# Kernel optimization log

Hardware: AMD Instinct MI355X
Metric: run time of the kernel (lower is better)

Reference implementation:

```python
import jax, jax.numpy as jnp
import numpy as np

D_MODEL = 1024
NUM_HEADS = 16
HEAD_DIM = D_MODEL // NUM_HEADS
B, TQ, TK = 4, 2048, 2048


def setup_inputs() -> dict:
    key = jax.random.key(0)
    ks = jax.random.split(key, 6)
    s = 1.0 / np.sqrt(D_MODEL)
    return {
        "x_q": jax.random.normal(ks[0], (B, TQ, D_MODEL), dtype=jnp.float32),
        "x_kv": jax.random.normal(ks[1], (B, TK, D_MODEL), dtype=jnp.float32),
        "attn_mask": jnp.zeros((TQ, TK), dtype=jnp.float32),
        "key_padding_mask": jnp.zeros((B, TK), dtype=bool),
        "Wq": jax.random.normal(ks[2], (D_MODEL, D_MODEL), dtype=jnp.float32) * s,
        "Wk": jax.random.normal(ks[3], (D_MODEL, D_MODEL), dtype=jnp.float32) * s,
        "Wv": jax.random.normal(ks[4], (D_MODEL, D_MODEL), dtype=jnp.float32) * s,
        "Wo": jax.random.normal(ks[5], (D_MODEL, D_MODEL), dtype=jnp.float32) * s,
    }


def reference(x_q, x_kv, attn_mask, key_padding_mask, Wq, Wk, Wv, Wo):
    b, tq, d = x_q.shape
    tk = x_kv.shape[1]
    h, hd = NUM_HEADS, HEAD_DIM
    # Linear(bias=False): y = x @ W.T ; split heads -> (b, h, t, hd)
    q = (x_q @ Wq.T).reshape(b, tq, h, hd).transpose(0, 2, 1, 3)
    k = (x_kv @ Wk.T).reshape(b, tk, h, hd).transpose(0, 2, 1, 3)
    v = (x_kv @ Wv.T).reshape(b, tk, h, hd).transpose(0, 2, 1, 3)
    scores = jnp.einsum("bhqd,bhkd->bhqk", q, k) / jnp.sqrt(jnp.float32(hd))
    scores = scores + attn_mask  # additive mask broadcasts over (b, h)
    scores = jnp.where(key_padding_mask[:, None, None, :], -jnp.inf, scores)
    w = jax.nn.softmax(scores, axis=-1)
    out = jnp.einsum("bhqk,bhkd->bhqd", w, v)  # (b, h, tq, hd)
    out = out.transpose(0, 2, 1, 3).reshape(b, tq, d)
    return out @ Wo.T
```

## Files before the change

### kernel.cpp

```cpp
#include <hip/hip_runtime.h>
#include <hip/hip_bf16.h>

#define TQ 2048
#define TKV 2048
#define NH 16
#define HD 64
#define DM 1024
#define BSZ 4
#define LDKV 2048

typedef __bf16 bf16_t;
typedef bf16_t bf16x8 __attribute__((ext_vector_type(8)));
typedef float f32x4 __attribute__((ext_vector_type(4)));

__device__ __forceinline__ f32x4 MFMA16(bf16x8 a, bf16x8 b, f32x4 c) {
  return __builtin_amdgcn_mfma_f32_16x16x32_bf16(a, b, c, 0, 0, 0);
}

__device__ __forceinline__ void gload_lds16(const void* g, void* l) {
  __builtin_amdgcn_global_load_lds((const __attribute__((address_space(1))) void*)g,
                                   (__attribute__((address_space(3))) void*)l,
                                   16, 0, 0);
}

__device__ __forceinline__ int vt_idx(int d, int k) {
  int bb = (k >> 3) ^ ((d >> 3) & 7) ^ (d & 7);
  return d * 64 + bb * 8 + (k & 7);
}
__device__ __forceinline__ int pl_idx(int q, int k) {
  int bb = (k >> 3) ^ (q & 7);
  return q * 64 + bb * 8 + (k & 7);
}

__global__ __launch_bounds__(256) void cvt_all(
    const float* __restrict__ xq, const float* __restrict__ xkv,
    const float* __restrict__ wq, const float* __restrict__ wk,
    const float* __restrict__ wv, const float* __restrict__ wo,
    bf16_t* __restrict__ oxq, bf16_t* __restrict__ oxkv,
    bf16_t* __restrict__ owq, bf16_t* __restrict__ owk,
    bf16_t* __restrict__ owv, bf16_t* __restrict__ owo) {
  const int blk = blockIdx.x;
  const float* src;
  bf16_t* dst;
  int base;
  if (blk < 4096)      { src = xq;  dst = oxq;  base = blk; }
  else if (blk < 8192) { src = xkv; dst = oxkv; base = blk - 4096; }
  else if (blk < 8704) { src = wq;  dst = owq;  base = blk - 8192; }
  else if (blk < 9216) { src = wk;  dst = owk;  base = blk - 8704; }
  else if (blk < 9728) { src = wv;  dst = owv;  base = blk - 9216; }
  else                 { src = wo;  dst = owo;  base = blk - 9728; }
  const int i = base * 256 + threadIdx.x;
  const float4* p = reinterpret_cast<const float4*>(src) + 2 * (size_t)i;
  float4 a = p[0], b = p[1];
  bf16x8 o;
  o[0] = (bf16_t)a.x; o[1] = (bf16_t)a.y; o[2] = (bf16_t)a.z; o[3] = (bf16_t)a.w;
  o[4] = (bf16_t)b.x; o[5] = (bf16_t)b.y; o[6] = (bf16_t)b.z; o[7] = (bf16_t)b.w;
  reinterpret_cast<bf16x8*>(dst)[i] = o;
}

template <bool BF16_OUT>
__global__ __launch_bounds__(256) void gemm_bt(const bf16_t* __restrict__ A,
                                               const bf16_t* __restrict__ Bw,
                                               void* __restrict__ Cout,
                                               int M, int N, int K, float scale) {
  __shared__ __align__(16) bf16_t As[128 * 32];
  __shared__ __align__(16) bf16_t Bs[128 * 32];
  const int tid = threadIdx.x;
  const int l = tid & 63;
  const int w = tid >> 6;
  const int wr = w >> 1, wc = w & 1;
  const int l15 = l & 15, lg = l >> 4;
  const long bm = (long)blockIdx.x * 128;
  const long bn = (long)blockIdx.y * 128;

  f32x4 acc[4][4] = {};

  const int c0i = tid, c1i = 256 + tid;
  const long ar0 = (bm + (c0i >> 2)) * (long)K + (c0i & 3) * 8;
  const long ar1 = (bm + (c1i >> 2)) * (long)K + (c1i & 3) * 8;
  const long br0 = (bn + (c0i >> 2)) * (long)K + (c0i & 3) * 8;
  const long br1 = (bn + (c1i >> 2)) * (long)K + (c1i & 3) * 8;

  for (int k0 = 0; k0 < K; k0 += 32) {
    __syncthreads();
    gload_lds16(A + ar0 + k0, As + c0i * 8);
    gload_lds16(A + ar1 + k0, As + c1i * 8);
    gload_lds16(Bw + br0 + k0, Bs + c0i * 8);
    gload_lds16(Bw + br1 + k0, Bs + c1i * 8);
    __syncthreads();

    bf16x8 af[4], bfr[4];
#pragma unroll
    for (int i = 0; i < 4; ++i)
      af[i] = *reinterpret_cast<const bf16x8*>(As + (wr * 64 + i * 16 + l15) * 32 + lg * 8);
#pragma unroll
    for (int j = 0; j < 4; ++j)
      bfr[j] = *reinterpret_cast<const bf16x8*>(Bs + (wc * 64 + j * 16 + l15) * 32 + lg * 8);
#pragma unroll
    for (int i = 0; i < 4; ++i)
#pragma unroll
      for (int j = 0; j < 4; ++j)
        acc[i][j] = MFMA16(af[i], bfr[j], acc[i][j]);
  }

#pragma unroll
  for (int i = 0; i < 4; ++i) {
#pragma unroll
    for (int j = 0; j < 4; ++j) {
#pragma unroll
      for (int r = 0; r < 4; ++r) {
        long rg = bm + wr * 64 + i * 16 + lg * 4 + r;
        long cg = bn + wc * 64 + j * 16 + l15;
        float v = acc[i][j][r] * scale;
        if (BF16_OUT)
          ((bf16_t*)Cout)[rg * N + cg] = (bf16_t)v;
        else
          ((float*)Cout)[rg * N + cg] = v;
      }
    }
  }
}

__global__ __launch_bounds__(256) void attn_fwd(const bf16_t* __restrict__ Qb,
                                                const bf16_t* __restrict__ KVb,
                                                const float* __restrict__ amask,
                                                const unsigned char* __restrict__ kpad,
                                                bf16_t* __restrict__ Ob) {
  __shared__ __align__(16) bf16_t Vt[64 * 64];
  __shared__ __align__(16) bf16_t Pl[4][16 * 64];
  const int tid = threadIdx.x;
  const int w = tid >> 6, l = tid & 63;
  const int l15 = l & 15, lg = l >> 4;
  const int b = blockIdx.y >> 4, h = blockIdx.y & 15;
  const int q0 = blockIdx.x * 64 + w * 16;
  const long qbase = (long)b * TQ * DM;
  const long kvbase = (long)b * TKV * LDKV;

  const bf16_t* qp = Qb + qbase + (long)(q0 + l15) * DM + h * HD + lg * 8;
  bf16x8 qf0 = *reinterpret_cast<const bf16x8*>(qp);
  bf16x8 qf1 = *reinterpret_cast<const bf16x8*>(qp + 32);

  f32x4 o[4] = {};
  float m[4], ls[4];
#pragma unroll
  for (int r = 0; r < 4; ++r) { m[r] = -1e30f; ls[r] = 0.f; }

  const int vrow = tid >> 3;
  const int dc = (tid & 7) * 8;

  for (int k0 = 0; k0 < TKV; k0 += 64) {
    __syncthreads();

    const bf16_t* vsrc = KVb + kvbase + (long)(k0 + vrow) * LDKV + 1024 + h * HD + dc;
    bf16x8 va = *reinterpret_cast<const bf16x8*>(vsrc);
    bf16x8 vb = *reinterpret_cast<const bf16x8*>(vsrc + 32 * LDKV);
#pragma unroll
    for (int j = 0; j < 8; ++j) {
      Vt[vt_idx(dc + j, vrow)] = va[j];
      Vt[vt_idx(dc + j, vrow + 32)] = vb[j];
    }

    f32x4 c[4] = {{0.f, 0.f, 0.f, 0.f}, {0.f, 0.f, 0.f, 0.f},
                  {0.f, 0.f, 0.f, 0.f}, {0.f, 0.f, 0.f, 0.f}};
#pragma unroll
    for (int f = 0; f < 4; ++f) {
      const bf16_t* kp = KVb + kvbase + (long)(k0 + 16 * f + l15) * LDKV + h * HD + lg * 8;
      bf16x8 ka = *reinterpret_cast<const bf16x8*>(kp);
      bf16x8 kb = *reinterpret_cast<const bf16x8*>(kp + 32);
      c[f] = MFMA16(qf0, ka, c[f]);
      c[f] = MFMA16(qf1, kb, c[f]);
    }

    __syncthreads();

    bool kpm[4];
#pragma unroll
    for (int f = 0; f < 4; ++f) kpm[f] = kpad[b * TKV + k0 + 16 * f + l15] != 0;

#pragma unroll
    for (int r = 0; r < 4; ++r) {
      const int qg = q0 + lg * 4 + r;
      const float* amrow = amask + (long)qg * TKV + k0;
      float s[4];
#pragma unroll
      for (int f = 0; f < 4; ++f) {
        s[f] = c[f][r] + amrow[16 * f + l15];
        if (kpm[f]) s[f] = -__builtin_inff();
      }
      float rmax = fmaxf(fmaxf(s[0], s[1]), fmaxf(s[2], s[3]));
#pragma unroll
      for (int d = 1; d < 16; d <<= 1) rmax = fmaxf(rmax, __shfl_xor(rmax, d, 64));
      const float mn = fmaxf(m[r], rmax);
      const float fac = __expf(m[r] - mn);
      float p[4], ps = 0.f;
#pragma unroll
      for (int f = 0; f < 4; ++f) { p[f] = __expf(s[f] - mn); ps += p[f]; }
#pragma unroll
      for (int d = 1; d < 16; d <<= 1) ps += __shfl_xor(ps, d, 64);
      ls[r] = ls[r] * fac + ps;
      m[r] = mn;
#pragma unroll
      for (int f = 0; f < 4; ++f) o[f][r] *= fac;
#pragma unroll
      for (int f = 0; f < 4; ++f)
        Pl[w][pl_idx(lg * 4 + r, 16 * f + l15)] = (bf16_t)p[f];
    }

#pragma unroll
    for (int hh = 0; hh < 2; ++hh) {
      bf16x8 pf = *reinterpret_cast<const bf16x8*>(&Pl[w][pl_idx(l15, hh * 32 + lg * 8)]);
#pragma unroll
      for (int f = 0; f < 4; ++f) {
        bf16x8 vf = *reinterpret_cast<const bf16x8*>(&Vt[vt_idx(16 * f + l15, hh * 32 + lg * 8)]);
        o[f] = MFMA16(pf, vf, o[f]);
      }
    }
  }

#pragma unroll
  for (int r = 0; r < 4; ++r) {
    const float inv = ls[r] > 0.f ? 1.f / ls[r] : 0.f;
    const long qg = q0 + lg * 4 + r;
    bf16_t* op = Ob + qbase + qg * DM + h * HD;
#pragma unroll
    for (int f = 0; f < 4; ++f) op[16 * f + l15] = (bf16_t)(o[f][r] * inv);
  }
}

extern "C" void kernel_launch(void* const* d_in, const int* in_sizes, int n_in,
                              void* d_out, int out_size, void* d_ws, size_t ws_size,
                              hipStream_t stream) {
  const float* x_q = (const float*)d_in[0];
  const float* x_kv = (const float*)d_in[1];
  const float* amask = (const float*)d_in[2];
  const unsigned char* kpad = (const unsigned char*)d_in[3];
  const float* Wq = (const float*)d_in[4];
  const float* Wk = (const float*)d_in[5];
  const float* Wv = (const float*)d_in[6];
  const float* Wo = (const float*)d_in[7];
  float* out = (float*)d_out;

  char* ws = (char*)d_ws;
  const size_t MB = 1024ull * 1024ull;
  bf16_t* xq_b  = (bf16_t*)(ws + 0 * MB);
  bf16_t* xkv_b = (bf16_t*)(ws + 16 * MB);
  bf16_t* Qb    = (bf16_t*)(ws + 32 * MB);
  bf16_t* KVb   = (bf16_t*)(ws + 48 * MB);
  bf16_t* Ob    = (bf16_t*)(ws + 80 * MB);
  bf16_t* Wq_b  = (bf16_t*)(ws + 96 * MB);
  bf16_t* Wk_b  = (bf16_t*)(ws + 98 * MB);
  bf16_t* Wv_b  = (bf16_t*)(ws + 100 * MB);
  bf16_t* Wo_b  = (bf16_t*)(ws + 102 * MB);

  const int NTOK = BSZ * TQ;

  cvt_all<<<10240, 256, 0, stream>>>(x_q, x_kv, Wq, Wk, Wv, Wo,
                                     xq_b, xkv_b, Wq_b, Wk_b, Wv_b, Wo_b);

  gemm_bt<true><<<dim3(NTOK / 128, DM / 128), 256, 0, stream>>>(
      xq_b, Wq_b, Qb, NTOK, DM, DM, 0.125f);
  gemm_bt<true><<<dim3(NTOK / 128, LDKV / 128), 256, 0, stream>>>(
      xkv_b, Wk_b, KVb, NTOK, LDKV, DM, 1.f);

  attn_fwd<<<dim3(TQ / 64, BSZ * NH), 256, 0, stream>>>(Qb, KVb, amask, kpad, Ob);

  gemm_bt<false><<<dim3(NTOK / 128, DM / 128), 256, 0, stream>>>(
      Ob, Wo_b, out, NTOK, DM, DM, 1.f);
}
```

Before: 588.5 us.

## Pre-transpose V and mask, use exp2 softmax, drop LDS V staging

The K/V projection now writes K and a transposed V (d-major per batch) directly from the GEMM epilogue, so the attention kernel reads V fragments straight from global memory instead of transposing through LDS with two block barriers per tile. The additive mask is pre-transposed to bf16 and scaled by log2(e), and key padding becomes a bf16 additive -inf vector. The log2(e) factor is also folded into the Q scale so softmax uses exp2f. Row sums are reduced across lanes only once at the end. In exchange there are extra preprocessing passes over the mask, and the mask is rounded to bf16.

```diff
diff --git a/kernel.cpp b/kernel.cpp
--- a/kernel.cpp
+++ b/kernel.cpp
@@ -7,10 +7,11 @@
 #define HD 64
 #define DM 1024
 #define BSZ 4
-#define LDKV 2048
+#define LOG2E 1.44269504088896340736f
 
 typedef __bf16 bf16_t;
 typedef bf16_t bf16x8 __attribute__((ext_vector_type(8)));
+typedef bf16_t bf16x4 __attribute__((ext_vector_type(4)));
 typedef float f32x4 __attribute__((ext_vector_type(4)));
 
 __device__ __forceinline__ f32x4 MFMA16(bf16x8 a, bf16x8 b, f32x4 c) {
@@ -23,10 +24,6 @@
                                    16, 0, 0);
 }
 
-__device__ __forceinline__ int vt_idx(int d, int k) {
-  int bb = (k >> 3) ^ ((d >> 3) & 7) ^ (d & 7);
-  return d * 64 + bb * 8 + (k & 7);
-}
 __device__ __forceinline__ int pl_idx(int q, int k) {
   int bb = (k >> 3) ^ (q & 7);
   return q * 64 + bb * 8 + (k & 7);
@@ -36,10 +33,22 @@
     const float* __restrict__ xq, const float* __restrict__ xkv,
     const float* __restrict__ wq, const float* __restrict__ wk,
     const float* __restrict__ wv, const float* __restrict__ wo,
+    const unsigned char* __restrict__ kpad,
     bf16_t* __restrict__ oxq, bf16_t* __restrict__ oxkv,
     bf16_t* __restrict__ owq, bf16_t* __restrict__ owk,
-    bf16_t* __restrict__ owv, bf16_t* __restrict__ owo) {
+    bf16_t* __restrict__ owv, bf16_t* __restrict__ owo,
+    bf16_t* __restrict__ okpd) {
   const int blk = blockIdx.x;
+  if (blk >= 10240) {
+    const int i = (blk - 10240) * 256 + threadIdx.x;
+    unsigned long long bits = *reinterpret_cast<const unsigned long long*>(kpad + (size_t)i * 8);
+    bf16x8 o;
+#pragma unroll
+    for (int j = 0; j < 8; ++j)
+      o[j] = ((bits >> (8 * j)) & 0xffull) ? (bf16_t)(-__builtin_inff()) : (bf16_t)0.f;
+    reinterpret_cast<bf16x8*>(okpd)[i] = o;
+    return;
+  }
   const float* src;
   bf16_t* dst;
   int base;
@@ -58,6 +67,29 @@
   reinterpret_cast<bf16x8*>(dst)[i] = o;
 }
 
+__global__ __launch_bounds__(256) void tmask(const float* __restrict__ am,
+                                             bf16_t* __restrict__ amt) {
+  __shared__ float T[64][65];
+  const int q0 = blockIdx.x * 64, k0 = blockIdx.y * 64;
+  const int tid = threadIdx.x;
+  const int r = tid >> 2, c4 = (tid & 3) * 4;
+#pragma unroll
+  for (int cc = 0; cc < 4; ++cc) {
+    const int kc = c4 + cc * 16;
+    float4 v = *reinterpret_cast<const float4*>(am + (long)(q0 + r) * TKV + k0 + kc);
+    T[kc + 0][r] = v.x; T[kc + 1][r] = v.y; T[kc + 2][r] = v.z; T[kc + 3][r] = v.w;
+  }
+  __syncthreads();
+  const int kr = tid >> 2, qc0 = (tid & 3) * 16;
+  bf16x8 o0, o1;
+#pragma unroll
+  for (int j = 0; j < 8; ++j) o0[j] = (bf16_t)(T[kr][qc0 + j] * LOG2E);
+#pragma unroll
+  for (int j = 0; j < 8; ++j) o1[j] = (bf16_t)(T[kr][qc0 + 8 + j] * LOG2E);
+  *reinterpret_cast<bf16x8*>(amt + (long)(k0 + kr) * TQ + q0 + qc0) = o0;
+  *reinterpret_cast<bf16x8*>(amt + (long)(k0 + kr) * TQ + q0 + qc0 + 8) = o1;
+}
+
 template <bool BF16_OUT>
 __global__ __launch_bounds__(256) void gemm_bt(const bf16_t* __restrict__ A,
                                                const bf16_t* __restrict__ Bw,
@@ -74,7 +106,6 @@
   const long bn = (long)blockIdx.y * 128;
 
   f32x4 acc[4][4] = {};
-
   const int c0i = tid, c1i = 256 + tid;
   const long ar0 = (bm + (c0i >> 2)) * (long)K + (c0i & 3) * 8;
   const long ar1 = (bm + (c1i >> 2)) * (long)K + (c1i & 3) * 8;
@@ -104,29 +135,97 @@
   }
 
 #pragma unroll
-  for (int i = 0; i < 4; ++i) {
-#pragma unroll
-    for (int j = 0; j < 4; ++j) {
+  for (int i = 0; i < 4; ++i)
+#pragma unroll
+    for (int j = 0; j < 4; ++j)
 #pragma unroll
       for (int r = 0; r < 4; ++r) {
         long rg = bm + wr * 64 + i * 16 + lg * 4 + r;
         long cg = bn + wc * 64 + j * 16 + l15;
         float v = acc[i][j][r] * scale;
-        if (BF16_OUT)
-          ((bf16_t*)Cout)[rg * N + cg] = (bf16_t)v;
-        else
-          ((float*)Cout)[rg * N + cg] = v;
+        if (BF16_OUT) ((bf16_t*)Cout)[rg * N + cg] = (bf16_t)v;
+        else          ((float*)Cout)[rg * N + cg] = v;
       }
-    }
+}
+
+__global__ __launch_bounds__(256) void gemm_kv(const bf16_t* __restrict__ A,
+                                               const bf16_t* __restrict__ Bw,
+                                               bf16_t* __restrict__ Kb,
+                                               bf16_t* __restrict__ VTb) {
+  __shared__ __align__(16) bf16_t As[128 * 32];
+  __shared__ __align__(16) bf16_t Bs[128 * 32];
+  const int K = DM;
+  const int tid = threadIdx.x;
+  const int l = tid & 63;
+  const int w = tid >> 6;
+  const int wr = w >> 1, wc = w & 1;
+  const int l15 = l & 15, lg = l >> 4;
+  const long bm = (long)blockIdx.x * 128;
+  const long bn = (long)blockIdx.y * 128;
+
+  f32x4 acc[4][4] = {};
+  const int c0i = tid, c1i = 256 + tid;
+  const long ar0 = (bm + (c0i >> 2)) * (long)K + (c0i & 3) * 8;
+  const long ar1 = (bm + (c1i >> 2)) * (long)K + (c1i & 3) * 8;
+  const long br0 = (bn + (c0i >> 2)) * (long)K + (c0i & 3) * 8;
+  const long br1 = (bn + (c1i >> 2)) * (long)K + (c1i & 3) * 8;
+
+  for (int k0 = 0; k0 < K; k0 += 32) {
+    __syncthreads();
+    gload_lds16(A + ar0 + k0, As + c0i * 8);
+    gload_lds16(A + ar1 + k0, As + c1i * 8);
+    gload_lds16(Bw + br0 + k0, Bs + c0i * 8);
+    gload_lds16(Bw + br1 + k0, Bs + c1i * 8);
+    __syncthreads();
+
+    bf16x8 af[4], bfr[4];
+#pragma unroll
+    for (int i = 0; i < 4; ++i)
+      af[i] = *reinterpret_cast<const bf16x8*>(As + (wr * 64 + i * 16 + l15) * 32 + lg * 8);
+#pragma unroll
+    for (int j = 0; j < 4; ++j)
+      bfr[j] = *reinterpret_cast<const bf16x8*>(Bs + (wc * 64 + j * 16 + l15) * 32 + lg * 8);
+#pragma unroll
+    for (int i = 0; i < 4; ++i)
+#pragma unroll
+      for (int j = 0; j < 4; ++j)
+        acc[i][j] = MFMA16(af[i], bfr[j], acc[i][j]);
+  }
+
+  if (bn < 1024) {
+#pragma unroll
+    for (int i = 0; i < 4; ++i)
+#pragma unroll
+      for (int j = 0; j < 4; ++j)
+#pragma unroll
+        for (int r = 0; r < 4; ++r) {
+          long rg = bm + wr * 64 + i * 16 + lg * 4 + r;
+          long cg = bn + wc * 64 + j * 16 + l15;
+          Kb[rg * DM + cg] = (bf16_t)acc[i][j][r];
+        }
+  } else {
+    const long brow = (bm >> 11) * (long)DM;
+    const long t0 = (bm & 2047);
+#pragma unroll
+    for (int i = 0; i < 4; ++i)
+#pragma unroll
+      for (int j = 0; j < 4; ++j) {
+        long d = bn - 1024 + wc * 64 + j * 16 + l15;
+        long t = t0 + wr * 64 + i * 16 + lg * 4;
+        bf16x4 pk;
+#pragma unroll
+        for (int r = 0; r < 4; ++r) pk[r] = (bf16_t)acc[i][j][r];
+        *reinterpret_cast<bf16x4*>(VTb + (brow + d) * TKV + t) = pk;
+      }
   }
 }
 
 __global__ __launch_bounds__(256) void attn_fwd(const bf16_t* __restrict__ Qb,
-                                                const bf16_t* __restrict__ KVb,
-                                                const float* __restrict__ amask,
-                                                const unsigned char* __restrict__ kpad,
+                                                const bf16_t* __restrict__ Kb,
+                                                const bf16_t* __restrict__ VTb,
+                                                const bf16_t* __restrict__ amt,
+                                                const bf16_t* __restrict__ kpd,
                                                 bf16_t* __restrict__ Ob) {
-  __shared__ __align__(16) bf16_t Vt[64 * 64];
   __shared__ __align__(16) bf16_t Pl[4][16 * 64];
   const int tid = threadIdx.x;
   const int w = tid >> 6, l = tid & 63;
@@ -134,76 +233,59 @@
   const int b = blockIdx.y >> 4, h = blockIdx.y & 15;
   const int q0 = blockIdx.x * 64 + w * 16;
   const long qbase = (long)b * TQ * DM;
-  const long kvbase = (long)b * TKV * LDKV;
 
   const bf16_t* qp = Qb + qbase + (long)(q0 + l15) * DM + h * HD + lg * 8;
   bf16x8 qf0 = *reinterpret_cast<const bf16x8*>(qp);
   bf16x8 qf1 = *reinterpret_cast<const bf16x8*>(qp + 32);
 
+  const bf16_t* kbase = Kb + qbase + h * HD;
+  const bf16_t* vbase = VTb + ((long)b * DM + h * HD) * (long)TKV;
+
   f32x4 o[4] = {};
   float m[4], ls[4];
 #pragma unroll
   for (int r = 0; r < 4; ++r) { m[r] = -1e30f; ls[r] = 0.f; }
 
-  const int vrow = tid >> 3;
-  const int dc = (tid & 7) * 8;
-
   for (int k0 = 0; k0 < TKV; k0 += 64) {
-    __syncthreads();
-
-    const bf16_t* vsrc = KVb + kvbase + (long)(k0 + vrow) * LDKV + 1024 + h * HD + dc;
-    bf16x8 va = *reinterpret_cast<const bf16x8*>(vsrc);
-    bf16x8 vb = *reinterpret_cast<const bf16x8*>(vsrc + 32 * LDKV);
-#pragma unroll
-    for (int j = 0; j < 8; ++j) {
-      Vt[vt_idx(dc + j, vrow)] = va[j];
-      Vt[vt_idx(dc + j, vrow + 32)] = vb[j];
+    bf16x4 mt[4];
+    float kpf[4];
+#pragma unroll
+    for (int f = 0; f < 4; ++f) {
+      mt[f] = *reinterpret_cast<const bf16x4*>(amt + (long)(k0 + 16 * f + l15) * TQ + q0 + lg * 4);
+      kpf[f] = (float)kpd[b * TKV + k0 + 16 * f + l15];
     }
 
-    f32x4 c[4] = {{0.f, 0.f, 0.f, 0.f}, {0.f, 0.f, 0.f, 0.f},
-                  {0.f, 0.f, 0.f, 0.f}, {0.f, 0.f, 0.f, 0.f}};
+    f32x4 c[4] = {};
 #pragma unroll
     for (int f = 0; f < 4; ++f) {
-      const bf16_t* kp = KVb + kvbase + (long)(k0 + 16 * f + l15) * LDKV + h * HD + lg * 8;
-      bf16x8 ka = *reinterpret_cast<const bf16x8*>(kp);
-      bf16x8 kb = *reinterpret_cast<const bf16x8*>(kp + 32);
-      c[f] = MFMA16(qf0, ka, c[f]);
-      c[f] = MFMA16(qf1, kb, c[f]);
+      const bf16_t* kp = kbase + (long)(k0 + 16 * f + l15) * DM + lg * 8;
+      c[f] = MFMA16(qf0, *reinterpret_cast<const bf16x8*>(kp), c[f]);
+      c[f] = MFMA16(qf1, *reinterpret_cast<const bf16x8*>(kp + 32), c[f]);
     }
 
-    __syncthreads();
-
-    bool kpm[4];
-#pragma unroll
-    for (int f = 0; f < 4; ++f) kpm[f] = kpad[b * TKV + k0 + 16 * f + l15] != 0;
-
 #pragma unroll
     for (int r = 0; r < 4; ++r) {
-      const int qg = q0 + lg * 4 + r;
-      const float* amrow = amask + (long)qg * TKV + k0;
-      float s[4];
-#pragma unroll
-      for (int f = 0; f < 4; ++f) {
-        s[f] = c[f][r] + amrow[16 * f + l15];
-        if (kpm[f]) s[f] = -__builtin_inff();
-      }
-      float rmax = fmaxf(fmaxf(s[0], s[1]), fmaxf(s[2], s[3]));
+      float s0 = c[0][r] + (float)mt[0][r] + kpf[0];
+      float s1 = c[1][r] + (float)mt[1][r] + kpf[1];
+      float s2 = c[2][r] + (float)mt[2][r] + kpf[2];
+      float s3 = c[3][r] + (float)mt[3][r] + kpf[3];
+      float rmax = fmaxf(fmaxf(s0, s1), fmaxf(s2, s3));
 #pragma unroll
       for (int d = 1; d < 16; d <<= 1) rmax = fmaxf(rmax, __shfl_xor(rmax, d, 64));
       const float mn = fmaxf(m[r], rmax);
-      const float fac = __expf(m[r] - mn);
-      float p[4], ps = 0.f;
-#pragma unroll
-      for (int f = 0; f < 4; ++f) { p[f] = __expf(s[f] - mn); ps += p[f]; }
-#pragma unroll
-      for (int d = 1; d < 16; d <<= 1) ps += __shfl_xor(ps, d, 64);
-      ls[r] = ls[r] * fac + ps;
+      const float fac = exp2f(m[r] - mn);
       m[r] = mn;
-#pragma unroll
-      for (int f = 0; f < 4; ++f) o[f][r] *= fac;
-#pragma unroll
-      for (int f = 0; f < 4; ++f)
-        Pl[w][pl_idx(lg * 4 + r, 16 * f + l15)] = (bf16_t)p[f];
+      const float p0 = exp2f(s0 - mn);
+      const float p1 = exp2f(s1 - mn);
+      const float p2 = exp2f(s2 - mn);
+      const float p3 = exp2f(s3 - mn);
+      ls[r] = ls[r] * fac + (p0 + p1 + p2 + p3);
+      o[0][r] *= fac; o[1][r] *= fac; o[2][r] *= fac; o[3][r] *= fac;
+      const int q = lg * 4 + r;
+      Pl[w][pl_idx(q, l15)]      = (bf16_t)p0;
+      Pl[w][pl_idx(q, 16 + l15)] = (bf16_t)p1;
+      Pl[w][pl_idx(q, 32 + l15)] = (bf16_t)p2;
+      Pl[w][pl_idx(q, 48 + l15)] = (bf16_t)p3;
     }
 
 #pragma unroll
@@ -211,19 +293,24 @@
       bf16x8 pf = *reinterpret_cast<const bf16x8*>(&Pl[w][pl_idx(l15, hh * 32 + lg * 8)]);
 #pragma unroll
       for (int f = 0; f < 4; ++f) {
-        bf16x8 vf = *reinterpret_cast<const bf16x8*>(&Vt[vt_idx(16 * f + l15, hh * 32 + lg * 8)]);
-        o[f] = MFMA16(pf, vf, o[f]);
+        const bf16_t* vp = vbase + (long)(16 * f + l15) * TKV + k0 + hh * 32 + lg * 8;
+        o[f] = MFMA16(pf, *reinterpret_cast<const bf16x8*>(vp), o[f]);
       }
     }
   }
 
 #pragma unroll
   for (int r = 0; r < 4; ++r) {
-    const float inv = ls[r] > 0.f ? 1.f / ls[r] : 0.f;
+    float t = ls[r];
+#pragma unroll
+    for (int d = 1; d < 16; d <<= 1) t += __shfl_xor(t, d, 64);
+    const float inv = t > 0.f ? 1.f / t : 0.f;
     const long qg = q0 + lg * 4 + r;
     bf16_t* op = Ob + qbase + qg * DM + h * HD;
-#pragma unroll
-    for (int f = 0; f < 4; ++f) op[16 * f + l15] = (bf16_t)(o[f][r] * inv);
+    op[l15]      = (bf16_t)(o[0][r] * inv);
+    op[16 + l15] = (bf16_t)(o[1][r] * inv);
+    op[32 + l15] = (bf16_t)(o[2][r] * inv);
+    op[48 + l15] = (bf16_t)(o[3][r] * inv);
   }
 }
 
@@ -242,27 +329,30 @@
 
   char* ws = (char*)d_ws;
   const size_t MB = 1024ull * 1024ull;
+  bf16_t* Ob    = (bf16_t*)(ws + 0 * MB);
   bf16_t* xq_b  = (bf16_t*)(ws + 0 * MB);
   bf16_t* xkv_b = (bf16_t*)(ws + 16 * MB);
   bf16_t* Qb    = (bf16_t*)(ws + 32 * MB);
-  bf16_t* KVb   = (bf16_t*)(ws + 48 * MB);
-  bf16_t* Ob    = (bf16_t*)(ws + 80 * MB);
-  bf16_t* Wq_b  = (bf16_t*)(ws + 96 * MB);
-  bf16_t* Wk_b  = (bf16_t*)(ws + 98 * MB);
-  bf16_t* Wv_b  = (bf16_t*)(ws + 100 * MB);
-  bf16_t* Wo_b  = (bf16_t*)(ws + 102 * MB);
+  bf16_t* Kb    = (bf16_t*)(ws + 48 * MB);
+  bf16_t* VTb   = (bf16_t*)(ws + 64 * MB);
+  bf16_t* amt   = (bf16_t*)(ws + 80 * MB);
+  bf16_t* Wq_b  = (bf16_t*)(ws + 88 * MB);
+  bf16_t* Wk_b  = (bf16_t*)(ws + 90 * MB);
+  bf16_t* Wv_b  = (bf16_t*)(ws + 92 * MB);
+  bf16_t* Wo_b  = (bf16_t*)(ws + 94 * MB);
+  bf16_t* kpdd  = (bf16_t*)(ws + 96 * MB);
 
   const int NTOK = BSZ * TQ;
 
-  cvt_all<<<10240, 256, 0, stream>>>(x_q, x_kv, Wq, Wk, Wv, Wo,
-                                     xq_b, xkv_b, Wq_b, Wk_b, Wv_b, Wo_b);
+  cvt_all<<<10244, 256, 0, stream>>>(x_q, x_kv, Wq, Wk, Wv, Wo, kpad,
+                                     xq_b, xkv_b, Wq_b, Wk_b, Wv_b, Wo_b, kpdd);
+  tmask<<<dim3(TQ / 64, TKV / 64), 256, 0, stream>>>(amask, amt);
 
   gemm_bt<true><<<dim3(NTOK / 128, DM / 128), 256, 0, stream>>>(
-      xq_b, Wq_b, Qb, NTOK, DM, DM, 0.125f);
-  gemm_bt<true><<<dim3(NTOK / 128, LDKV / 128), 256, 0, stream>>>(
-      xkv_b, Wk_b, KVb, NTOK, LDKV, DM, 1.f);
-
-  attn_fwd<<<dim3(TQ / 64, BSZ * NH), 256, 0, stream>>>(Qb, KVb, amask, kpad, Ob);
+      xq_b, Wq_b, Qb, NTOK, DM, DM, 0.125f * LOG2E);
+  gemm_kv<<<dim3(NTOK / 128, 2 * DM / 128), 256, 0, stream>>>(xkv_b, Wk_b, Kb, VTb);
+
+  attn_fwd<<<dim3(TQ / 64, BSZ * NH), 256, 0, stream>>>(Qb, Kb, VTb, amt, kpdd, Ob);
 
   gemm_bt<false><<<dim3(NTOK / 128, DM / 128), 256, 0, stream>>>(
       Ob, Wo_b, out, NTOK, DM, DM, 1.f);
```

Measured after the change: 819.9 us. +39.3%, slower.
